# Performance work log

Hardware: AMD Instinct MI355X
Metric: run time of the kernel (lower is better)

Reference implementation:

```python
import jax, jax.numpy as jnp
import numpy as np

EMBED_DIM = 1024
NUM_HEADS = 16
HEAD_DIM = EMBED_DIM // NUM_HEADS


def setup_inputs() -> dict:
    key = jax.random.key(0)
    ks = jax.random.split(key, 11)
    B, S, D = 2, 2048, EMBED_DIM
    s = 1.0 / np.sqrt(D)
    inp = {
        "query": jax.random.normal(ks[0], (B, S, D), jnp.float32),
        "key": jax.random.normal(ks[1], (B, S, D), jnp.float32),
        "value": jax.random.normal(ks[2], (B, S, D), jnp.float32),
        # torch Linear weights: [out, in]
        "Wq": jax.random.normal(ks[3], (D, D), jnp.float32) * s,
        "bq": jnp.zeros((D,), jnp.float32),
        "Wk": jax.random.normal(ks[4], (D, D), jnp.float32) * s,
        "bk": jnp.zeros((D,), jnp.float32),
        "Wv": jax.random.normal(ks[5], (D, D), jnp.float32) * s,
        "bv": jnp.zeros((D,), jnp.float32),
        "Wo": jax.random.normal(ks[6], (D, D), jnp.float32) * s,
        "bo": jnp.zeros((D,), jnp.float32),
    }
    return inp


def reference(query, key, value, Wq, bq, Wk, bk, Wv, bv, Wo, bo):
    B, Q, D = query.shape
    K = key.shape[1]
    H, Hd = NUM_HEADS, HEAD_DIM
    # NOTE: source divides by scaling = head_dim**-0.5, i.e. multiplies by sqrt(head_dim)
    scaling = float(Hd) ** (-0.5)

    q = (query @ Wq.T + bq).reshape(B, Q, H, Hd).transpose(0, 2, 1, 3)  # [B,H,Q,Hd]
    k = (key @ Wk.T + bk).reshape(B, K, H, Hd).transpose(0, 2, 1, 3)    # [B,H,K,Hd]
    v = (value @ Wv.T + bv).reshape(B, K, H, Hd).transpose(0, 2, 1, 3)  # [B,H,K,Hd]

    scores = jnp.einsum("bhqd,bhkd->bhqk", q, k) / scaling
    attn = jax.nn.softmax(scores, axis=-1)  # dropout=0 (eval)
    out = jnp.einsum("bhqk,bhkd->bhqd", attn, v)
    out = out.transpose(0, 2, 1, 3).reshape(B, Q, D)
    return out @ Wo.T + bo
```

## Files before the change

### kernel.cpp

```cpp
#include <hip/hip_runtime.h>
#include <type_traits>
#include <utility>

#define B_ 2
#define S_ 2048
#define D_ 1024
#define H_ 16
#define HD_ 64
#define KDIM 1024

typedef __attribute__((ext_vector_type(8))) short    s16x8;
typedef __attribute__((ext_vector_type(8))) _Float16 h16x8;
typedef __attribute__((ext_vector_type(4))) float    f32x4;
typedef __attribute__((ext_vector_type(16))) float   f32x16;
typedef __attribute__((ext_vector_type(4))) int      i32x4;
typedef __attribute__((ext_vector_type(2))) int      i32x2;

template <typename T, typename = void> struct mfma_takes : std::false_type {};
template <typename T>
struct mfma_takes<T, std::void_t<decltype(__builtin_amdgcn_mfma_f32_16x16x32_f16(
    std::declval<T>(), std::declval<T>(), std::declval<f32x4>(), 0, 0, 0))>>
    : std::true_type {};
using frag8 = std::conditional_t<mfma_takes<h16x8>::value, h16x8, s16x8>;

__device__ __forceinline__ f32x4 mfma_f16(frag8 a, frag8 b, f32x4 c) {
  return __builtin_amdgcn_mfma_f32_16x16x32_f16(a, b, c, 0, 0, 0);
}
__device__ __forceinline__ f32x16 mfma32(frag8 a, frag8 b, f32x16 c) {
  return __builtin_amdgcn_mfma_f32_32x32x16_f16(a, b, c, 0, 0, 0);
}

__device__ __forceinline__ short f2h(float f) {
  _Float16 h = (_Float16)f;
  short s; __builtin_memcpy(&s, &h, 2);
  return s;
}
__device__ __forceinline__ int pk2h(float a, float b) {
  auto p = __builtin_amdgcn_cvt_pkrtz(a, b);
  int r; __builtin_memcpy(&r, &p, 4); return r;
}
__device__ __forceinline__ frag8 ld_frag(const short* p) {
  return __builtin_bit_cast(frag8, *(const i32x4*)p);
}
__device__ __forceinline__ float fast_exp2(float x) {
  return __builtin_amdgcn_exp2f(x);
}
__device__ __forceinline__ void pl32swap(int& a, int& b) {
  asm volatile("v_permlane32_swap_b32 %0, %1" : "+v"(a), "+v"(b));
}

typedef __attribute__((address_space(1))) const void gvoid;
typedef __attribute__((address_space(3))) void lvoid;
__device__ __forceinline__ void async_copy16(const void* g, void* l) {
  __builtin_amdgcn_global_load_lds((gvoid*)g, (lvoid*)l, 16, 0, 0);
}

#define RAW_BARRIER() asm volatile("s_barrier" ::: "memory")
#define WAITCNT_VM(n) asm volatile("s_waitcnt vmcnt(" #n ")" ::: "memory")

__global__ __launch_bounds__(256)
void conv_all(const float* __restrict__ q, const float* __restrict__ k,
              const float* __restrict__ v, const float* __restrict__ Wq,
              const float* __restrict__ Wk, const float* __restrict__ Wv,
              const float* __restrict__ Wo,
              short* __restrict__ qh, short* __restrict__ kh,
              short* __restrict__ vh, short* __restrict__ wq,
              short* __restrict__ wk, short* __restrict__ wv,
              short* __restrict__ wo) {
  const int blk = blockIdx.x;
  const float* src; short* dst; int base;
  if (blk < 2048)      { src = q;  dst = qh; base = blk; }
  else if (blk < 4096) { src = k;  dst = kh; base = blk - 2048; }
  else if (blk < 6144) { src = v;  dst = vh; base = blk - 4096; }
  else if (blk < 6656) { src = Wq; dst = wq; base = blk - 6144; }
  else if (blk < 7168) { src = Wk; dst = wk; base = blk - 6656; }
  else if (blk < 7680) { src = Wv; dst = wv; base = blk - 7168; }
  else                 { src = Wo; dst = wo; base = blk - 7680; }
  const int i = base * 2048 + threadIdx.x * 8;
  float4 a0 = *(const float4*)(src + i);
  float4 a1 = *(const float4*)(src + i + 4);
  short h[8] = { f2h(a0.x), f2h(a0.y), f2h(a0.z), f2h(a0.w),
                 f2h(a1.x), f2h(a1.y), f2h(a1.z), f2h(a1.w) };
  i32x4 ph; __builtin_memcpy(&ph, h, 16);
  *(i32x4*)(dst + i) = ph;
}

__global__ __launch_bounds__(256, 3)
void gemm_qkv(const short* __restrict__ qh, const short* __restrict__ kh,
              const short* __restrict__ vh, const short* __restrict__ wq,
              const short* __restrict__ wk, const short* __restrict__ wv,
              const float* __restrict__ bq, const float* __restrict__ bk,
              const float* __restrict__ bv, short* __restrict__ Qf,
              short* __restrict__ Kf, short* __restrict__ Vt, float QS) {
  __shared__ short As[3 * 4096];
  __shared__ short Bs[3 * 4096];

  const int blk = blockIdx.x;
  const int xcd = blk & 7, i = blk >> 3;
  const int p = (i >> 3) * 8 + xcd;
  const int bn = i & 7;
  const int z = p >> 5, bm = p & 31;
  const short* Ap = z == 0 ? qh : z == 1 ? kh : vh;
  const short* Wp = z == 0 ? wq : z == 1 ? wk : wv;
  const float* bias = z == 0 ? bq : z == 1 ? bk : bv;
  short* Out = z == 0 ? Qf : z == 1 ? Kf : Vt;
  const float scale = z == 0 ? QS : 1.0f;
  const int omode = z == 2 ? 2 : 1;

  const int t = threadIdx.x, wave = t >> 6, lane = t & 63;
  const int laneN = lane & 15, quad = lane >> 4;
  const int wm = wave & 1, wn = wave >> 1;

  f32x4 acc[4][4];
#pragma unroll
  for (int i2 = 0; i2 < 4; ++i2)
#pragma unroll
    for (int j = 0; j < 4; ++j)
#pragma unroll
      for (int r = 0; r < 4; ++r) acc[i2][j][r] = 0.f;

  auto stage = [&](int buf, int kk) {
#pragma unroll
    for (int j = 0; j < 2; ++j) {
      const int chunk = j * 256 + t;
      const int row = chunk >> 2;
      const int gg = (chunk & 3) ^ ((row >> 1) & 3);
      async_copy16(Ap + (size_t)(bm * 128 + row) * KDIM + kk + gg * 8,
                   As + buf * 4096 + chunk * 8);
      async_copy16(Wp + (size_t)(bn * 128 + row) * KDIM + kk + gg * 8,
                   Bs + buf * 4096 + chunk * 8);
    }
  };

  stage(0, 0);
  stage(1, 32);
  int buf = 0;
  for (int kk = 0; kk < KDIM; kk += 32) {
    if (kk + 64 < KDIM) {
      int nb = buf + 2; if (nb >= 3) nb -= 3;
      stage(nb, kk + 64);
      WAITCNT_VM(8);
    } else if (kk + 32 < KDIM) {
      WAITCNT_VM(4);
    } else {
      WAITCNT_VM(0);
    }
    RAW_BARRIER();

    frag8 aF[4], bF[4];
#pragma unroll
    for (int mi = 0; mi < 4; ++mi) {
      const int row = wm * 64 + mi * 16 + laneN;
      aF[mi] = ld_frag(As + buf * 4096 + row * 32 +
                       ((quad ^ ((row >> 1) & 3)) * 8));
    }
#pragma unroll
    for (int ni = 0; ni < 4; ++ni) {
      const int row = wn * 64 + ni * 16 + laneN;
      bF[ni] = ld_frag(Bs + buf * 4096 + row * 32 +
                       ((quad ^ ((row >> 1) & 3)) * 8));
    }
#pragma unroll
    for (int mi = 0; mi < 4; ++mi)
#pragma unroll
      for (int ni = 0; ni < 4; ++ni)
        acc[mi][ni] = mfma_f16(aF[mi], bF[ni], acc[mi][ni]);
    RAW_BARRIER();
    buf = buf + 1 == 3 ? 0 : buf + 1;
  }

  short* scr = As + wave * 1152;
  const int h = bn * 2 + wn;
  if (omode == 2) {
    const int bidx = bm >> 4;
    const int sbase = (bm * 128 + wm * 64) & 2047;
#pragma unroll
    for (int ni = 0; ni < 4; ++ni) {
      const float bb = bias[bn * 128 + wn * 64 + ni * 16 + laneN];
#pragma unroll
      for (int mi = 0; mi < 4; ++mi) {
        short pk[4];
#pragma unroll
        for (int r = 0; r < 4; ++r) pk[r] = f2h(acc[mi][ni][r] + bb);
        i32x2 w; __builtin_memcpy(&w, pk, 8);
        *(i32x2*)(scr + laneN * 72 + mi * 16 + quad * 4) = w;
      }
#pragma unroll
      for (int j = 0; j < 2; ++j) {
        const int ff = lane * 2 + j, hdr = ff >> 3, ch = ff & 7;
        i32x4 v = *(const i32x4*)(scr + hdr * 72 + ch * 8);
        *(i32x4*)(Vt + (((size_t)(bidx * H_ + h)) * HD_ + ni * 16 + hdr) * S_ +
                  sbase + ch * 8) = v;
      }
    }
  } else {
#pragma unroll
    for (int mi = 0; mi < 4; ++mi) {
#pragma unroll
      for (int ni = 0; ni < 4; ++ni) {
        const float bb = bias[bn * 128 + wn * 64 + ni * 16 + laneN];
#pragma unroll
        for (int r = 0; r < 4; ++r)
          scr[(quad * 4 + r) * 72 + ni * 16 + laneN] =
              f2h((acc[mi][ni][r] + bb) * scale);
      }
#pragma unroll
      for (int j = 0; j < 2; ++j) {
        const int ff = lane * 2 + j, row = ff >> 3, ch = ff & 7;
        const int rowg = bm * 128 + wm * 64 + mi * 16 + row;
        const int bidx = rowg >> 11, s = rowg & 2047;
        i32x4 v = *(const i32x4*)(scr + row * 72 + ch * 8);
        *(i32x4*)(Out + (((size_t)(bidx * H_ + h)) * S_ + s) * HD_ + ch * 8) = v;
      }
    }
  }
}

__global__ __launch_bounds__(256, 3)
void gemm_out(const short* __restrict__ Ap, const short* __restrict__ Wp,
              const float* __restrict__ bias, float* __restrict__ Out) {
  __shared__ short As[2 * 8192];
  __shared__ short Bs[2 * 4096];
  const int blk = blockIdx.x;
  const int xcd = blk & 7, i = blk >> 3;
  const int bm = (i >> 4) * 8 + xcd;
  const int bn = i & 15;

  const int t = threadIdx.x, wave = t >> 6, lane = t & 63;
  const int laneN = lane & 15, quad = lane >> 4;
  const int wm = wave & 1, wn = wave >> 1;

  f32x4 acc[4][2];
#pragma unroll
  for (int i2 = 0; i2 < 4; ++i2)
#pragma unroll
    for (int j = 0; j < 2; ++j)
#pragma unroll
      for (int r = 0; r < 4; ++r) acc[i2][j][r] = 0.f;

  auto stage = [&](int buf, int kk) {
#pragma unroll
    for (int j = 0; j < 4; ++j) {
      const int c = j * 256 + t;
      const int row = c >> 3, g = (c & 7) ^ (row & 7);
      async_copy16(Ap + (size_t)(bm * 128 + row) * KDIM + kk + g * 8,
                   As + buf * 8192 + c * 8);
    }
#pragma unroll
    for (int j = 0; j < 2; ++j) {
      const int c = j * 256 + t;
      const int row = c >> 3, g = (c & 7) ^ (row & 7);
      async_copy16(Wp + (size_t)(bn * 64 + row) * KDIM + kk + g * 8,
                   Bs + buf * 4096 + c * 8);
    }
  };

  int offA[4][2], offB[2][2];
#pragma unroll
  for (int mi = 0; mi < 4; ++mi) {
    const int row = wm * 64 + mi * 16 + laneN;
#pragma unroll
    for (int ks = 0; ks < 2; ++ks)
      offA[mi][ks] = row * 64 + (((quad + 4 * ks) ^ (row & 7)) * 8);
  }
#pragma unroll
  for (int ni = 0; ni < 2; ++ni) {
    const int row = wn * 32 + ni * 16 + laneN;
#pragma unroll
    for (int ks = 0; ks < 2; ++ks)
      offB[ni][ks] = row * 64 + (((quad + 4 * ks) ^ (row & 7)) * 8);
  }

  stage(0, 0);
  int buf = 0;
  for (int kk = 0; kk < KDIM; kk += 64) {
    if (kk + 64 < KDIM) {
      stage(buf ^ 1, kk + 64);
      WAITCNT_VM(6);
    } else {
      WAITCNT_VM(0);
    }
    RAW_BARRIER();

    frag8 aF[4][2], bF[2][2];
#pragma unroll
    for (int mi = 0; mi < 4; ++mi) {
      aF[mi][0] = ld_frag(As + buf * 8192 + offA[mi][0]);
      aF[mi][1] = ld_frag(As + buf * 8192 + offA[mi][1]);
    }
#pragma unroll
    for (int ni = 0; ni < 2; ++ni) {
      bF[ni][0] = ld_frag(Bs + buf * 4096 + offB[ni][0]);
      bF[ni][1] = ld_frag(Bs + buf * 4096 + offB[ni][1]);
    }
#pragma unroll
    for (int mi = 0; mi < 4; ++mi)
#pragma unroll
      for (int ni = 0; ni < 2; ++ni) {
        acc[mi][ni] = mfma_f16(aF[mi][0], bF[ni][0], acc[mi][ni]);
        acc[mi][ni] = mfma_f16(aF[mi][1], bF[ni][1], acc[mi][ni]);
      }
    RAW_BARRIER();
    buf ^= 1;
  }

  float* scr = (float*)As + wave * 576;
#pragma unroll
  for (int mi = 0; mi < 4; ++mi) {
#pragma unroll
    for (int ni = 0; ni < 2; ++ni) {
      const float bb = bias[bn * 64 + wn * 32 + ni * 16 + laneN];
#pragma unroll
      for (int r = 0; r < 4; ++r)
        scr[(quad * 4 + r) * 36 + ni * 16 + laneN] = acc[mi][ni][r] + bb;
    }
#pragma unroll
    for (int j = 0; j < 2; ++j) {
      const int ff = lane * 2 + j, row = ff >> 3, ch = ff & 7;
      const int rowg = bm * 128 + wm * 64 + mi * 16 + row;
      f32x4 v = *(const f32x4*)(scr + row * 36 + ch * 4);
      *(f32x4*)(Out + (size_t)rowg * 1024 + bn * 64 + wn * 32 + ch * 4) = v;
    }
  }
}

__global__ __launch_bounds__(256, 2)
void attn(const short* __restrict__ Qf, const short* __restrict__ Kf,
          const short* __restrict__ Vt_, short* __restrict__ Ow) {
  __shared__ short Ks[4 * 4096];
  __shared__ short Vts[4 * 4096];

  const int blk = blockIdx.x;
  const int xcd = blk & 7, local = blk >> 3;
  const int pair = xcd * 4 + (local >> 4);
  const int h = pair & 15, b = pair >> 4, qt = local & 15;
  const size_t head = ((size_t)b * H_ + h) * (size_t)S_ * HD_;

  const int t = threadIdx.x;
  const int wave = t >> 6, lane = t & 63;
  const int l31 = lane & 31, hi = lane >> 5;

  const int q0 = qt * 128 + wave * 32;

  frag8 qf[4];
  {
    const short* qp = Qf + head + (size_t)(q0 + l31) * HD_ + hi * 8;
#pragma unroll
    for (int ds = 0; ds < 4; ++ds) qf[ds] = ld_frag(qp + ds * 16);
  }

  f32x16 o0, o1;
#pragma unroll
  for (int r = 0; r < 16; ++r) { o0[r] = 0.f; o1[r] = 0.f; }
  float m_r = -1e30f, l_r = 0.f;

  const int c0 = t, c1 = 256 + t;
  const int r0 = c0 >> 3, gg0 = (c0 & 7) ^ (r0 & 7);
  const int r1 = c1 >> 3, gg1 = (c1 & 7) ^ (r1 & 7);
  const short* kp0 = Kf + head + (size_t)r0 * HD_ + gg0 * 8;
  const short* kp1 = Kf + head + (size_t)r1 * HD_ + gg1 * 8;
  const short* vp0 = Vt_ + head + (size_t)r0 * S_ + gg0 * 8;
  const short* vp1 = Vt_ + head + (size_t)r1 * S_ + gg1 * 8;
  const int d0 = c0 * 8, d1 = c1 * 8;

  int off2[2][4];
#pragma unroll
  for (int hf = 0; hf < 2; ++hf) {
    const int row = hf * 32 + l31;
#pragma unroll
    for (int j = 0; j < 4; ++j)
      off2[hf][j] = row * 64 + (((j * 2 + hi) ^ (row & 7)) * 8);
  }

  async_copy16(kp0, Ks + d0);  async_copy16(kp1, Ks + d1);
  async_copy16(vp0, Vts + d0); async_copy16(vp1, Vts + d1);
  kp0 += 4096; kp1 += 4096; vp0 += 64; vp1 += 64;
  async_copy16(kp0, Ks + 4096 + d0);  async_copy16(kp1, Ks + 4096 + d1);
  async_copy16(vp0, Vts + 4096 + d0); async_copy16(vp1, Vts + 4096 + d1);
  kp0 += 4096; kp1 += 4096; vp0 += 64; vp1 += 64;

#define ATTN_TILE(B0, STG)                                                   \
  {                                                                          \
    if (STG == 1) {                                                          \
      const int nb = ((B0) + 2) & 3;                                         \
      async_copy16(kp0, Ks + nb * 4096 + d0);                                \
      async_copy16(kp1, Ks + nb * 4096 + d1);                                \
      async_copy16(vp0, Vts + nb * 4096 + d0);                               \
      async_copy16(vp1, Vts + nb * 4096 + d1);                               \
      kp0 += 4096; kp1 += 4096; vp0 += 64; vp1 += 64;                        \
      WAITCNT_VM(8);                                                         \
    } else if (STG == 2) {                                                   \
      WAITCNT_VM(4);                                                         \
    } else {                                                                 \
      WAITCNT_VM(0);                                                         \
    }                                                                        \
    RAW_BARRIER();                                                           \
    const short* KbS = Ks + (B0) * 4096;                                     \
    const short* VbS = Vts + (B0) * 4096;                                    \
                  \
    f32x16 sA, sB;                                                           \
    _Pragma("unroll")                                                        \
    for (int r = 0; r < 16; ++r) { sA[r] = 0.f; sB[r] = 0.f; }               \
    __builtin_amdgcn_s_setprio(1);                                           \
    _Pragma("unroll")                                                        \
    for (int ds = 0; ds < 4; ++ds) {                                         \
      frag8 ka = ld_frag(KbS + off2[0][ds]);                                 \
      frag8 kb = ld_frag(KbS + off2[1][ds]);                                 \
      sA = mfma32(ka, qf[ds], sA);                                           \
      sB = mfma32(kb, qf[ds], sB);                                           \
    }                                                                        \
    __builtin_amdgcn_s_setprio(0);                                           \
                 \
    {                                                                        \
      float mA = sA[0], mB = sB[0];                                          \
      _Pragma("unroll")                                                      \
      for (int r = 1; r < 16; ++r) {                                         \
        mA = fmaxf(mA, sA[r]); mB = fmaxf(mB, sB[r]);                        \
      }                                                                      \
      float mx = fmaxf(mA, mB);                                              \
      mx = fmaxf(mx, __shfl_xor(mx, 32));                                    \
      if (__any(mx > m_r + 8.f)) {                                           \
        const float mn = fmaxf(m_r, mx);                                     \
        const float al = fast_exp2(m_r - mn);                                \
        m_r = mn; l_r *= al;                                                 \
        _Pragma("unroll")                                                    \
        for (int r = 0; r < 16; ++r) { o0[r] *= al; o1[r] *= al; }           \
      }                                                                      \
      float rs = 0.f;                                                        \
      _Pragma("unroll")                                                      \
      for (int r = 0; r < 16; ++r) {                                         \
        const float pa = fast_exp2(sA[r] - m_r);                             \
        const float pb = fast_exp2(sB[r] - m_r);                             \
        sA[r] = pa; sB[r] = pb; rs += pa + pb;                               \
      }                                                                      \
      rs += __shfl_xor(rs, 32);                                              \
      l_r += rs;                                                             \
    }                                                                        \
       \
    frag8 pf0, pf1, pf2, pf3;                                                \
    {                                                                        \
      int w0, w1, w2, w3; i32x4 fw;                                          \
      w0 = pk2h(sA[0], sA[1]);   w1 = pk2h(sA[2], sA[3]);                    \
      w2 = pk2h(sA[4], sA[5]);   w3 = pk2h(sA[6], sA[7]);                    \
      pl32swap(w0, w2); pl32swap(w1, w3);                                    \
      fw[0] = w0; fw[1] = w1; fw[2] = w2; fw[3] = w3;                        \
      pf0 = __builtin_bit_cast(frag8, fw);                                   \
      w0 = pk2h(sA[8], sA[9]);   w1 = pk2h(sA[10], sA[11]);                  \
      w2 = pk2h(sA[12], sA[13]); w3 = pk2h(sA[14], sA[15]);                  \
      pl32swap(w0, w2); pl32swap(w1, w3);                                    \
      fw[0] = w0; fw[1] = w1; fw[2] = w2; fw[3] = w3;                        \
      pf1 = __builtin_bit_cast(frag8, fw);                                   \
      w0 = pk2h(sB[0], sB[1]);   w1 = pk2h(sB[2], sB[3]);                    \
      w2 = pk2h(sB[4], sB[5]);   w3 = pk2h(sB[6], sB[7]);                    \
      pl32swap(w0, w2); pl32swap(w1, w3);                                    \
      fw[0] = w0; fw[1] = w1; fw[2] = w2; fw[3] = w3;                        \
      pf2 = __builtin_bit_cast(frag8, fw);                                   \
      w0 = pk2h(sB[8], sB[9]);   w1 = pk2h(sB[10], sB[11]);                  \
      w2 = pk2h(sB[12], sB[13]); w3 = pk2h(sB[14], sB[15]);                  \
      pl32swap(w0, w2); pl32swap(w1, w3);                                    \
      fw[0] = w0; fw[1] = w1; fw[2] = w2; fw[3] = w3;                        \
      pf3 = __builtin_bit_cast(frag8, fw);                                   \
    }                                                                        \
                        \
    __builtin_amdgcn_s_setprio(1);                                           \
    {                                                                        \
      frag8 va, vb;                                                          \
      va = ld_frag(VbS + off2[0][0]); o0 = mfma32(va, pf0, o0);              \
      vb = ld_frag(VbS + off2[1][0]); o1 = mfma32(vb, pf0, o1);              \
      va = ld_frag(VbS + off2[0][1]); o0 = mfma32(va, pf1, o0);              \
      vb = ld_frag(VbS + off2[1][1]); o1 = mfma32(vb, pf1, o1);              \
      va = ld_frag(VbS + off2[0][2]); o0 = mfma32(va, pf2, o0);              \
      vb = ld_frag(VbS + off2[1][2]); o1 = mfma32(vb, pf2, o1);              \
      va = ld_frag(VbS + off2[0][3]); o0 = mfma32(va, pf3, o0);              \
      vb = ld_frag(VbS + off2[1][3]); o1 = mfma32(vb, pf3, o1);              \
    }                                                                        \
    __builtin_amdgcn_s_setprio(0);                                           \
  }

  for (int it = 0; it < 7; ++it) {
    ATTN_TILE(0, 1)
    ATTN_TILE(1, 1)
    ATTN_TILE(2, 1)
    ATTN_TILE(3, 1)
  }
  ATTN_TILE(0, 1)
  ATTN_TILE(1, 1)
  ATTN_TILE(2, 2)
  ATTN_TILE(3, 0)
#undef ATTN_TILE

  {
    const float inv = 1.0f / l_r;
    short* dst = Ow + ((size_t)b * S_ + q0 + l31) * D_ + h * HD_ + hi * 4;
#pragma unroll
    for (int rg = 0; rg < 4; ++rg) {
      i32x2 w;
      w[0] = pk2h(o0[rg * 4 + 0] * inv, o0[rg * 4 + 1] * inv);
      w[1] = pk2h(o0[rg * 4 + 2] * inv, o0[rg * 4 + 3] * inv);
      *(i32x2*)(dst + rg * 8) = w;
      i32x2 w2;
      w2[0] = pk2h(o1[rg * 4 + 0] * inv, o1[rg * 4 + 1] * inv);
      w2[1] = pk2h(o1[rg * 4 + 2] * inv, o1[rg * 4 + 3] * inv);
      *(i32x2*)(dst + 32 + rg * 8) = w2;
    }
  }
}

extern "C" void kernel_launch(void* const* d_in, const int* in_sizes, int n_in,
                              void* d_out, int out_size, void* d_ws, size_t ws_size,
                              hipStream_t stream) {
  const float* q  = (const float*)d_in[0];
  const float* k  = (const float*)d_in[1];
  const float* v  = (const float*)d_in[2];
  const float* Wq = (const float*)d_in[3];
  const float* bq = (const float*)d_in[4];
  const float* Wk = (const float*)d_in[5];
  const float* bk = (const float*)d_in[6];
  const float* Wv = (const float*)d_in[7];
  const float* bv = (const float*)d_in[8];
  const float* Wo = (const float*)d_in[9];
  const float* bo = (const float*)d_in[10];

  const size_t NTOK = (size_t)B_ * S_ * D_;
  const size_t NW   = (size_t)D_ * D_;
  short* p = (short*)d_ws;
  short* qh = p; p += NTOK;  short* kh = p; p += NTOK;  short* vh = p; p += NTOK;
  short* wq = p; p += NW;    short* wk = p; p += NW;
  short* wv = p; p += NW;    short* wo = p; p += NW;
  short* Qf = p; p += NTOK;  short* Kf = p; p += NTOK;
  short* Vt = p; p += NTOK;  short* Ow = p; p += NTOK;

  dim3 blk(256);

  conv_all<<<8192, blk, 0, stream>>>(q, k, v, Wq, Wk, Wv, Wo,
                                     qh, kh, vh, wq, wk, wv, wo);

  const float QS = 11.541560327111707f;
  gemm_qkv<<<768, blk, 0, stream>>>(qh, kh, vh, wq, wk, wv, bq, bk, bv,
                                    Qf, Kf, Vt, QS);

  attn<<<512, dim3(256), 0, stream>>>(Qf, Kf, Vt, Ow);

  gemm_out<<<512, blk, 0, stream>>>(Ow, wo, bo, (float*)d_out);
}
```

Before: 222.4 us.

## Fuse fp32-to-fp16 activation conversion into QKV GEMM A-tile staging

The separate conversion pass over the query/key/value activations is removed. The QKV GEMM now loads fp32 A tiles into registers, converts them to fp16 and writes them into the LDS ring one stage ahead, while the weight tiles still use async global-to-LDS copies. This avoids writing and re-reading the fp16 activation copies (about 25 MB of traffic) and shrinks the conversion launch. In exchange, every GEMM block reads twice as many bytes for A, repeated across the N tiles, and the A prefetch now uses registers and VALU conversion work in the main loop.

```diff
diff --git a/kernel.cpp b/kernel.cpp
--- a/kernel.cpp
+++ b/kernel.cpp
@@ -59,23 +59,16 @@
 #define WAITCNT_VM(n) asm volatile("s_waitcnt vmcnt(" #n ")" ::: "memory")
 
 __global__ __launch_bounds__(256)
-void conv_all(const float* __restrict__ q, const float* __restrict__ k,
-              const float* __restrict__ v, const float* __restrict__ Wq,
-              const float* __restrict__ Wk, const float* __restrict__ Wv,
-              const float* __restrict__ Wo,
-              short* __restrict__ qh, short* __restrict__ kh,
-              short* __restrict__ vh, short* __restrict__ wq,
-              short* __restrict__ wk, short* __restrict__ wv,
-              short* __restrict__ wo) {
+void conv_w(const float* __restrict__ Wq, const float* __restrict__ Wk,
+            const float* __restrict__ Wv, const float* __restrict__ Wo,
+            short* __restrict__ wq, short* __restrict__ wk,
+            short* __restrict__ wv, short* __restrict__ wo) {
   const int blk = blockIdx.x;
   const float* src; short* dst; int base;
-  if (blk < 2048)      { src = q;  dst = qh; base = blk; }
-  else if (blk < 4096) { src = k;  dst = kh; base = blk - 2048; }
-  else if (blk < 6144) { src = v;  dst = vh; base = blk - 4096; }
-  else if (blk < 6656) { src = Wq; dst = wq; base = blk - 6144; }
-  else if (blk < 7168) { src = Wk; dst = wk; base = blk - 6656; }
-  else if (blk < 7680) { src = Wv; dst = wv; base = blk - 7168; }
-  else                 { src = Wo; dst = wo; base = blk - 7680; }
+  if (blk < 512)        { src = Wq; dst = wq; base = blk; }
+  else if (blk < 1024)  { src = Wk; dst = wk; base = blk - 512; }
+  else if (blk < 1536)  { src = Wv; dst = wv; base = blk - 1024; }
+  else                  { src = Wo; dst = wo; base = blk - 1536; }
   const int i = base * 2048 + threadIdx.x * 8;
   float4 a0 = *(const float4*)(src + i);
   float4 a1 = *(const float4*)(src + i + 4);
@@ -86,8 +79,8 @@
 }
 
 __global__ __launch_bounds__(256, 3)
-void gemm_qkv(const short* __restrict__ qh, const short* __restrict__ kh,
-              const short* __restrict__ vh, const short* __restrict__ wq,
+void gemm_qkv(const float* __restrict__ Aq, const float* __restrict__ Ak,
+              const float* __restrict__ Av, const short* __restrict__ wq,
               const short* __restrict__ wk, const short* __restrict__ wv,
               const float* __restrict__ bq, const float* __restrict__ bk,
               const float* __restrict__ bv, short* __restrict__ Qf,
@@ -100,7 +93,7 @@
   const int p = (i >> 3) * 8 + xcd;
   const int bn = i & 7;
   const int z = p >> 5, bm = p & 31;
-  const short* Ap = z == 0 ? qh : z == 1 ? kh : vh;
+  const float* Af = z == 0 ? Aq : z == 1 ? Ak : Av;
   const short* Wp = z == 0 ? wq : z == 1 ? wk : wv;
   const float* bias = z == 0 ? bq : z == 1 ? bk : bv;
   short* Out = z == 0 ? Qf : z == 1 ? Kf : Vt;
@@ -119,29 +112,65 @@
 #pragma unroll
       for (int r = 0; r < 4; ++r) acc[i2][j][r] = 0.f;
 
-  auto stage = [&](int buf, int kk) {
+  const int ch0 = t, ch1 = 256 + t;
+  const int ar0 = ch0 >> 2, ag0 = (ch0 & 3) ^ ((ar0 >> 1) & 3);
+  const int ar1 = ch1 >> 2, ag1 = (ch1 & 3) ^ ((ar1 >> 1) & 3);
+  const float* ap0 = Af + (size_t)(bm * 128 + ar0) * KDIM + ag0 * 8;
+  const float* ap1 = Af + (size_t)(bm * 128 + ar1) * KDIM + ag1 * 8;
+
+  f32x4 rA0a, rA0b, rA1a, rA1b;
+
+  auto loadA = [&](int kk) {
+    rA0a = *(const f32x4*)(ap0 + kk);
+    rA0b = *(const f32x4*)(ap0 + kk + 4);
+    rA1a = *(const f32x4*)(ap1 + kk);
+    rA1b = *(const f32x4*)(ap1 + kk + 4);
+  };
+  auto writeA = [&](int slot) {
+    short pk[8];
+    pk[0] = f2h(rA0a[0]); pk[1] = f2h(rA0a[1]);
+    pk[2] = f2h(rA0a[2]); pk[3] = f2h(rA0a[3]);
+    pk[4] = f2h(rA0b[0]); pk[5] = f2h(rA0b[1]);
+    pk[6] = f2h(rA0b[2]); pk[7] = f2h(rA0b[3]);
+    i32x4 w0; __builtin_memcpy(&w0, pk, 16);
+    *(i32x4*)(As + slot * 4096 + ch0 * 8) = w0;
+    pk[0] = f2h(rA1a[0]); pk[1] = f2h(rA1a[1]);
+    pk[2] = f2h(rA1a[2]); pk[3] = f2h(rA1a[3]);
+    pk[4] = f2h(rA1b[0]); pk[5] = f2h(rA1b[1]);
+    pk[6] = f2h(rA1b[2]); pk[7] = f2h(rA1b[3]);
+    i32x4 w1; __builtin_memcpy(&w1, pk, 16);
+    *(i32x4*)(As + slot * 4096 + ch1 * 8) = w1;
+  };
+  auto stageB = [&](int slot, int kk) {
 #pragma unroll
     for (int j = 0; j < 2; ++j) {
       const int chunk = j * 256 + t;
       const int row = chunk >> 2;
       const int gg = (chunk & 3) ^ ((row >> 1) & 3);
-      async_copy16(Ap + (size_t)(bm * 128 + row) * KDIM + kk + gg * 8,
-                   As + buf * 4096 + chunk * 8);
       async_copy16(Wp + (size_t)(bn * 128 + row) * KDIM + kk + gg * 8,
-                   Bs + buf * 4096 + chunk * 8);
+                   Bs + slot * 4096 + chunk * 8);
     }
   };
 
-  stage(0, 0);
-  stage(1, 32);
+  loadA(0);
+  writeA(0);
+  loadA(32);
+  stageB(0, 0);
+  stageB(1, 32);
+
   int buf = 0;
   for (int kk = 0; kk < KDIM; kk += 32) {
     if (kk + 64 < KDIM) {
+      WAITCNT_VM(2);
+      int ns = buf + 1; if (ns >= 3) ns -= 3;
+      writeA(ns);
+      loadA(kk + 64);
       int nb = buf + 2; if (nb >= 3) nb -= 3;
-      stage(nb, kk + 64);
-      WAITCNT_VM(8);
+      stageB(nb, kk + 64);
     } else if (kk + 32 < KDIM) {
-      WAITCNT_VM(4);
+      WAITCNT_VM(2);
+      int ns = buf + 1; if (ns >= 3) ns -= 3;
+      writeA(ns);
     } else {
       WAITCNT_VM(0);
     }
@@ -524,7 +553,6 @@
   const size_t NTOK = (size_t)B_ * S_ * D_;
   const size_t NW   = (size_t)D_ * D_;
   short* p = (short*)d_ws;
-  short* qh = p; p += NTOK;  short* kh = p; p += NTOK;  short* vh = p; p += NTOK;
   short* wq = p; p += NW;    short* wk = p; p += NW;
   short* wv = p; p += NW;    short* wo = p; p += NW;
   short* Qf = p; p += NTOK;  short* Kf = p; p += NTOK;
@@ -532,11 +560,10 @@
 
   dim3 blk(256);
 
-  conv_all<<<8192, blk, 0, stream>>>(q, k, v, Wq, Wk, Wv, Wo,
-                                     qh, kh, vh, wq, wk, wv, wo);
+  conv_w<<<2048, blk, 0, stream>>>(Wq, Wk, Wv, Wo, wq, wk, wv, wo);
 
   const float QS = 11.541560327111707f;
-  gemm_qkv<<<768, blk, 0, stream>>>(qh, kh, vh, wq, wk, wv, bq, bk, bv,
+  gemm_qkv<<<768, blk, 0, stream>>>(q, k, v, wq, wk, wv, bq, bk, bv,
                                     Qf, Kf, Vt, QS);
 
   attn<<<512, dim3(256), 0, stream>>>(Qf, Kf, Vt, Ow);
```

Result: slower. 233.9 us (+5.2%).
